# Performance work log

Hardware: AMD Instinct MI355X
Metric: run time of the kernel (lower is better)

The kernel has to match this reference:

```python
import jax, jax.numpy as jnp
import numpy as np

# blueprint: (root_input_idx, children) where child >= 0 -> input[child], child < 0 -> hidden[-child-1]
BLUEPRINT = [(0, [0, 1, 2, 3]), (4, [4, 5, 6, 7]), (8, [8, 9, 10, 11]), (12, [12, 13, 14, 15]), (0, [-1, -2, -3, -4])]
B, T, V, E, H, TAGS = 32768, 16, 32000, 32, 64, 64


def setup_inputs() -> dict:
    key = jax.random.key(0)
    ks = jax.random.split(key, 13)
    x = jax.random.randint(ks[0], (B, T), 0, V)  # token ids (never hit pad row V)
    s = jax.random.randint(ks[1], (B,), 1, 5)    # lengths in [1, 4]
    sc = 0.125  # ~1/sqrt(H), matches torch LSTM uniform init scale
    emb = (jax.random.normal(ks[2], (V + 1, E), dtype=jnp.float32) * 0.1).at[V].set(0.0)
    Wih = jax.random.uniform(ks[3], (4 * H, E), minval=-sc, maxval=sc, dtype=jnp.float32)
    Whh = jax.random.uniform(ks[4], (4 * H, H), minval=-sc, maxval=sc, dtype=jnp.float32)
    bih = jax.random.uniform(ks[5], (4 * H,), minval=-sc, maxval=sc, dtype=jnp.float32)
    bhh = jax.random.uniform(ks[6], (4 * H,), minval=-sc, maxval=sc, dtype=jnp.float32)
    h0 = jax.random.uniform(ks[7], (H,), minval=-1.0, maxval=1.0, dtype=jnp.float32)
    c0 = jax.random.uniform(ks[8], (H,), minval=-1.0, maxval=1.0, dtype=jnp.float32)
    Wc = jax.random.uniform(ks[9], (E, H + E), minval=-0.1, maxval=0.1, dtype=jnp.float32)
    bc = jnp.zeros((E,), dtype=jnp.float32)
    Wt = jax.random.uniform(ks[10], (TAGS, E), minval=-0.18, maxval=0.18, dtype=jnp.float32)
    bt = jnp.zeros((TAGS,), dtype=jnp.float32)
    return {"x": x, "s": s, "emb": emb, "Wih": Wih, "Whh": Whh, "bih": bih, "bhh": bhh,
            "h0": h0, "c0": c0, "Wc": Wc, "bc": bc, "Wt": Wt, "bt": bt}


def _lstm_seq(cseq, h0b, c0b, Wih, Whh, b):
    # cseq: [B, L, E] -> outputs [B, L, H]; torch gate order i, f, g, o
    def step(carry, xt):
        h, cc = carry
        g = xt @ Wih.T + h @ Whh.T + b
        i, f, gg, o = jnp.split(g, 4, axis=-1)
        cc = jax.nn.sigmoid(f) * cc + jax.nn.sigmoid(i) * jnp.tanh(gg)
        h = jax.nn.sigmoid(o) * jnp.tanh(cc)
        return (h, cc), h
    _, hs = jax.lax.scan(step, (h0b, c0b), jnp.swapaxes(cseq, 0, 1))
    return jnp.swapaxes(hs, 0, 1)


def reference(x, s, emb, Wih, Whh, bih, bhh, h0, c0, Wc, bc, Wt, bt):
    bsz = x.shape[0]
    inputs = emb[x]  # [B, T, E]
    h0b = jnp.broadcast_to(h0[None, :], (bsz, h0.shape[0]))
    c0b = jnp.broadcast_to(c0[None, :], (bsz, c0.shape[0]))
    b = bih + bhh
    hidden = []
    for root, children in BLUEPRINT:
        r = inputs[:, root]  # [B, E]
        ch = [inputs[:, c] if c >= 0 else hidden[-c - 1] for c in children]
        cseq = jnp.stack(ch, axis=1)  # [B, L, E]
        L = cseq.shape[1]
        o = _lstm_seq(cseq, h0b, c0b, Wih, Whh, b)  # [B, L, H]
        # pack/pad semantics: positions t >= s[b] are zero after pad_packed; relu(0)=0
        mask = (jnp.arange(L)[None, :] < s[:, None]).astype(o.dtype)
        o = jax.nn.relu(o) * mask[..., None]
        last = o[:, -1]  # [B, H] (zero where s[b] < L, matching torch)
        comb = jax.nn.relu(jnp.concatenate([r, last], axis=1) @ Wc.T + bc)  # [B, E]
        hidden.append(comb)
    logits = hidden[-1] @ Wt.T + bt  # [B, TAGS]
    return jax.nn.log_softmax(logits, axis=1)
```

## Files before the change

### kernel.cpp

```cpp
#include <hip/hip_runtime.h>

#define NB 32768
#define NT 16
#define NV 32001
#define NE 32
#define NTAGS 64

typedef __attribute__((ext_vector_type(8))) short short8;
typedef __attribute__((ext_vector_type(4))) float f4;

#define MFMA16(a, b, c) __builtin_amdgcn_mfma_f32_16x16x32_bf16(a, b, c, 0, 0, 0)
#define CFENCE() asm volatile("" ::: "memory")
#define LDSSYNC() asm volatile("s_waitcnt lgkmcnt(0)" ::: "memory")

__device__ __forceinline__ float sigm_(float x) {
    return __builtin_amdgcn_rcpf(1.0f + __expf(-x));
}
__device__ __forceinline__ float tanh2_(float x) {
    float e = __expf(-2.0f * x);
    return fmaf(2.0f, __builtin_amdgcn_rcpf(1.0f + e), -1.0f);
}
__device__ __forceinline__ short f2bf(float x) {
    union { float f; unsigned u; } v; v.f = x;
    unsigned r = v.u + 0x7fffu + ((v.u >> 16) & 1u);
    return (short)(r >> 16);
}

__global__ __launch_bounds__(1024) void classify_prep(
    const int* __restrict__ s, const float* __restrict__ emb,
    const float* __restrict__ Wih, const float* __restrict__ Whh,
    const float* __restrict__ bih, const float* __restrict__ bhh,
    const float* __restrict__ Wc, const float* __restrict__ Wt,
    short* __restrict__ embH, short* __restrict__ wpack, short* __restrict__ wc1,
    short* __restrict__ wc2, short* __restrict__ wth, float* __restrict__ bsum,
    int* __restrict__ cH, int* __restrict__ listH, int* __restrict__ listL) {
    __shared__ int wbH[16], wbL[16];
    const int tid = threadIdx.x, b = blockIdx.x;
    if (b < 32) {
        const int row = b * 1024 + tid;
        const bool heavy = s[row] >= 4;
        unsigned long long mk = __ballot(heavy);
        const int wv = tid >> 6, ln = tid & 63;
        if (ln == 0) wbH[wv] = __popcll(mk);
        __syncthreads();
        if (tid == 0) {
            int tH = 0, tL = 0;
#pragma unroll
            for (int i = 0; i < 16; ++i) {
                int ch = wbH[i];
                wbH[i] = tH; wbL[i] = tL;
                tH += ch; tL += 64 - ch;
            }
            cH[b] = tH;
        }
        __syncthreads();
        unsigned long long ltm = (1ull << ln) - 1ull;
        if (heavy) listH[b * 1024 + wbH[wv] + __popcll(mk & ltm)] = row;
        else       listL[b * 1024 + wbL[wv] + __popcll((~mk) & ltm)] = row;
    }
    for (int i = b * 1024 + tid; i < NV * NE; i += 262144) embH[i] = f2bf(emb[i]);
    if (b == 32) {
        for (int t = tid; t < 18432; t += 1024) {
            int r = t / 72, c = t % 72;
            wpack[t] = f2bf(c < 64 ? Whh[r * 64 + c] : 0.f);
        }
        for (int t = tid; t < 10240; t += 1024) {
            int r = t / 40, c = t % 40;
            wpack[18432 + t] = f2bf(c < 32 ? Wih[r * 32 + c] : 0.f);
        }
        if (tid < 1024) { int r = tid >> 5, c = tid & 31; wc1[tid] = f2bf(Wc[r * 96 + c]); }
        for (int t = tid; t < 2048; t += 1024) {
            int r = t >> 6, c = t & 63;
            wc2[t] = f2bf(Wc[r * 96 + 32 + c]);
        }
        for (int t = tid; t < 2048; t += 1024) {
            int r = t >> 5, c = t & 31;
            wth[t] = f2bf(Wt[r * 32 + c]);
        }
        if (tid < 256) bsum[tid] = bih[tid] + bhh[tid];
    }
}

__global__ __launch_bounds__(256, 2) void main_fused(
    const int* __restrict__ x, const float* __restrict__ emb,
    const float* __restrict__ h0, const float* __restrict__ c0,
    const float* __restrict__ Wc, const float* __restrict__ bc,
    const float* __restrict__ Wt, const float* __restrict__ bt,
    const float* __restrict__ bsum,
    const short* __restrict__ wpack, const short* __restrict__ wc1,
    const short* __restrict__ wc2, const short* __restrict__ wth,
    const short* __restrict__ embH, const int* __restrict__ cH,
    const int* __restrict__ listH, const int* __restrict__ listL,
    float* __restrict__ out) {
    __shared__ __align__(16) short sWhh[18432];
    __shared__ __align__(16) short sWih[10240];
    __shared__ __align__(16) short sHA[4][16 * 72];
    __shared__ __align__(16) short sCmb[4][16 * 40];
    __shared__ __align__(16) short sC4[4][4 * 40];
    __shared__ int sRow[16];

    const int tid = threadIdx.x, wave = tid >> 6, lane = tid & 63;
    const int q = lane >> 4, n = lane & 15;
    const int NW = gridDim.x * 4;
    const int gw = blockIdx.x * 4 + wave;

    int cs = (lane < 32) ? cH[lane] : 0;
    int v = cs;
#pragma unroll
    for (int o = 1; o < 32; o <<= 1) { int t2 = __shfl_up(v, o); if (lane >= o) v += t2; }
    const int vIncl = v, vExcl = v - cs;
    const int nH = __shfl(vIncl, 31);
    const int nL = NB - nH;
    const int liIncl = (lane + 1) * 1024 - vIncl;
    const int liExcl = lane * 1024 - vExcl;
    const int nHB = (nH + 15) >> 4;
    const bool heavyBlk = (int)blockIdx.x < nHB;

    if (heavyBlk) {
        for (int i = tid; i < 2304; i += 256)
            ((uint4*)sWhh)[i] = ((const uint4*)wpack)[i];
        for (int i = tid; i < 1280; i += 256)
            ((uint4*)sWih)[i] = ((const uint4*)(wpack + 18432))[i];
        __syncthreads();
    }

    if (heavyBlk) {
        short* hA = sHA[wave];
        short* cmbB = sCmb[0];
        short* c4 = sC4[0];

        float bias16[16];
#pragma unroll
        for (int tl = 0; tl < 16; ++tl) bias16[tl] = bsum[tl * 16 + n];
        float bc2[2] = {bc[n], bc[16 + n]};
        float bt4[4] = {bt[n], bt[16 + n], bt[32 + n], bt[48 + n]};
        float c0v[4];
#pragma unroll
        for (int u = 0; u < 4; ++u) c0v[u] = c0[u * 16 + n];
        short8 h0f0, h0f1;
#pragma unroll
        for (int j = 0; j < 8; ++j) {
            h0f0[j] = f2bf(h0[q * 8 + j]);
            h0f1[j] = f2bf(h0[32 + q * 8 + j]);
        }
        const float c0w = c0[wave * 16 + n];

        const f4 zero4 = {0.f, 0.f, 0.f, 0.f};
        f4 acc[16];
        float cst[4][4];

        auto doStep = [&](short8 aP, short8 ah0, short8 ah1, bool doRelu) {
#pragma unroll
            for (int tl = 0; tl < 16; ++tl)
                acc[tl] = MFMA16(aP, *(const short8*)&sWih[(tl * 16 + n) * 40 + q * 8], zero4);
#pragma unroll
            for (int tl = 0; tl < 16; ++tl) {
                const short* rbp = &sWhh[(tl * 16 + n) * 72 + q * 8];
                f4 t0 = acc[tl];
                t0 = MFMA16(ah0, *(const short8*)rbp, t0);
                t0 = MFMA16(ah1, *(const short8*)(rbp + 32), t0);
                acc[tl] = t0;
            }
            CFENCE();
#pragma unroll
            for (int u = 0; u < 4; ++u)
#pragma unroll
                for (int r = 0; r < 4; ++r) {
                    float ip = acc[u][r] + bias16[u];
                    float fp = acc[4 + u][r] + bias16[4 + u];
                    float gp = acc[8 + u][r] + bias16[8 + u];
                    float op = acc[12 + u][r] + bias16[12 + u];
                    float cc = fmaf(sigm_(fp), cst[r][u], sigm_(ip) * tanh2_(gp));
                    cst[r][u] = cc;
                    float hh = sigm_(op) * tanh2_(cc);
                    if (doRelu) hh = fmaxf(hh, 0.f);
                    hA[(q * 4 + r) * 72 + u * 16 + n] = f2bf(hh);
                }
            CFENCE();
        };

#pragma unroll 1
        for (int itb = blockIdx.x; itb * 16 < nH; itb += (int)gridDim.x) {
            const int base = itb * 16;
            int idxq = min(base + wave * 4 + q, nH - 1);
            int sl = 0;
#pragma unroll
            for (int b2 = 0; b2 < 32; ++b2) sl += (__shfl(vIncl, b2) <= idxq) ? 1 : 0;
            const int row = listH[sl * 1024 + idxq - __shfl(vExcl, sl)];
            if (n == 0) sRow[wave * 4 + q] = row;
            const int tokAll = x[row * 16 + n];
            const int liBase = (n & 3) * 16 + (n >> 2) * 4;

#pragma unroll
            for (int u = 0; u < 4; ++u)
#pragma unroll
                for (int r = 0; r < 4; ++r) cst[r][u] = c0v[u];
            const int tokR0 = __shfl(tokAll, liBase);
            short8 aNext = *(const short8*)&embH[tokR0 * 32 + q * 8];
            short8 a0 = h0f0, a1 = h0f1;
#pragma unroll 1
            for (int t = 0; t < 4; ++t) {
                short8 aP = aNext;
                if (t < 3) {
                    int tk2 = __shfl(tokAll, liBase + t + 1);
                    aNext = *(const short8*)&embH[tk2 * 32 + q * 8];
                }
                doStep(aP, a0, a1, t == 3);
                if (t < 3) {
                    a0 = *(const short8*)&hA[n * 72 + q * 8];
                    a1 = *(const short8*)&hA[n * 72 + 32 + q * 8];
                }
            }
            {
                short8 aRoot = *(const short8*)&embH[tokR0 * 32 + q * 8];
                short8 lh0 = *(const short8*)&hA[n * 72 + q * 8];
                short8 lh1 = *(const short8*)&hA[n * 72 + 32 + q * 8];
#pragma unroll
                for (int tl2 = 0; tl2 < 2; ++tl2) {
                    float bv = bc2[tl2];
                    f4 t0 = {bv, bv, bv, bv};
                    short8 b1 = *(const short8*)&wc1[(tl2 * 16 + n) * 32 + q * 8];
                    t0 = MFMA16(aRoot, b1, t0);
                    const short* rbp = &wc2[(tl2 * 16 + n) * 64 + q * 8];
                    t0 = MFMA16(lh0, *(const short8*)rbp, t0);
                    t0 = MFMA16(lh1, *(const short8*)(rbp + 32), t0);
#pragma unroll
                    for (int r = 0; r < 4; ++r) {
                        int m = q * 4 + r;
                        cmbB[((m >> 2) * 16 + wave * 4 + (m & 3)) * 40 + tl2 * 16 + n] =
                            f2bf(fmaxf(t0[r], 0.f));
                    }
                }
            }
            __syncthreads();

            float bias4[4];
#pragma unroll
            for (int j = 0; j < 4; ++j) bias4[j] = bsum[(j * 4 + wave) * 16 + n];
            float cstw[4] = {c0w, c0w, c0w, c0w};
            short8 b0 = h0f0, b1 = h0f1;
            f4 ac4[4];
#pragma unroll
            for (int t = 0; t < 4; ++t) {
                short* hbw = (t & 1) ? sHA[1] : sHA[0];
                short8 aC = *(const short8*)&cmbB[(t * 16 + n) * 40 + q * 8];
#pragma unroll
                for (int j = 0; j < 4; ++j)
                    ac4[j] = MFMA16(aC,
                        *(const short8*)&sWih[((j * 4 + wave) * 16 + n) * 40 + q * 8], zero4);
#pragma unroll
                for (int j = 0; j < 4; ++j) {
                    const short* rbp = &sWhh[((j * 4 + wave) * 16 + n) * 72 + q * 8];
                    f4 t0 = ac4[j];
                    t0 = MFMA16(b0, *(const short8*)rbp, t0);
                    t0 = MFMA16(b1, *(const short8*)(rbp + 32), t0);
                    ac4[j] = t0;
                }
                CFENCE();
#pragma unroll
                for (int r = 0; r < 4; ++r) {
                    float ip = ac4[0][r] + bias4[0];
                    float fp = ac4[1][r] + bias4[1];
                    float gp = ac4[2][r] + bias4[2];
                    float op = ac4[3][r] + bias4[3];
                    float cc = fmaf(sigm_(fp), cstw[r], sigm_(ip) * tanh2_(gp));
                    cstw[r] = cc;
                    float hh = sigm_(op) * tanh2_(cc);
                    if (t == 3) hh = fmaxf(hh, 0.f);
                    hbw[(q * 4 + r) * 72 + wave * 16 + n] = f2bf(hh);
                }
                CFENCE();
                __syncthreads();
                if (t < 3) {
                    b0 = *(const short8*)&hbw[n * 72 + q * 8];
                    b1 = *(const short8*)&hbw[n * 72 + 32 + q * 8];
                }
            }

            {
                const short* hL = sHA[1];
                int rv = sRow[n];
                int tokR = x[rv * 16];
                short8 aR = *(const short8*)&embH[tokR * 32 + q * 8];
                short8 lb0 = *(const short8*)&hL[n * 72 + q * 8];
                short8 lb1 = *(const short8*)&hL[n * 72 + 32 + q * 8];
#pragma unroll
                for (int tl2 = 0; tl2 < 2; ++tl2) {
                    float bv = bc2[tl2];
                    f4 t0 = {bv, bv, bv, bv};
                    short8 b1f = *(const short8*)&wc1[(tl2 * 16 + n) * 32 + q * 8];
                    t0 = MFMA16(aR, b1f, t0);
                    const short* rbp = &wc2[(tl2 * 16 + n) * 64 + q * 8];
                    t0 = MFMA16(lb0, *(const short8*)rbp, t0);
                    t0 = MFMA16(lb1, *(const short8*)(rbp + 32), t0);
                    if (q == wave) {
#pragma unroll
                        for (int r = 0; r < 4; ++r)
                            c4[(wave * 4 + r) * 40 + tl2 * 16 + n] = f2bf(fmaxf(t0[r], 0.f));
                    }
                }
            }
            __syncthreads();

            {
                short8 cA = *(const short8*)&c4[n * 40 + q * 8];
                f4 a3[4];
#pragma unroll
                for (int tl3 = 0; tl3 < 4; ++tl3) {
                    float bv = bt4[tl3];
                    f4 t0 = {bv, bv, bv, bv};
                    short8 bW = *(const short8*)&wth[(tl3 * 16 + n) * 32 + q * 8];
                    a3[tl3] = MFMA16(cA, bW, t0);
                }
#pragma unroll
                for (int r = 0; r < 4; ++r) {
                    float l0 = a3[0][r], l1 = a3[1][r], l2 = a3[2][r], l3 = a3[3][r];
                    float mx = fmaxf(fmaxf(l0, l1), fmaxf(l2, l3));
#pragma unroll
                    for (int o2 = 8; o2; o2 >>= 1) mx = fmaxf(mx, __shfl_xor(mx, o2));
                    float sm = __expf(l0 - mx) + __expf(l1 - mx) +
                               __expf(l2 - mx) + __expf(l3 - mx);
#pragma unroll
                    for (int o2 = 8; o2; o2 >>= 1) sm += __shfl_xor(sm, o2);
                    float lse = mx + __logf(sm);
                    if (q == wave && base + wave * 4 + r < nH) {
                        int ro = sRow[wave * 4 + r];
                        out[ro * 64 + n] = l0 - lse;
                        out[ro * 64 + 16 + n] = l1 - lse;
                        out[ro * 64 + 32 + n] = l2 - lse;
                        out[ro * 64 + 48 + n] = l3 - lse;
                    }
                }
            }
        }
    }

    if (nL > 0) {
        const int nLB = max((int)gridDim.x - nHB, 0);
        int lw, nlw;
        if (nLB > 0) {
            if (heavyBlk) { lw = -1; nlw = 0; }
            else { lw = ((int)blockIdx.x - nHB) * 4 + wave; nlw = nLB * 4; }
        } else {
            lw = NW - 1 - gw; nlw = NW;
        }
        if (lw >= 0) {
            short* cmbL = sCmb[wave];
            f4 bcV[2], btV[4];
#pragma unroll
            for (int t = 0; t < 2; ++t) { float bv = bc[t * 16 + n]; bcV[t] = f4{bv, bv, bv, bv}; }
#pragma unroll
            for (int t = 0; t < 4; ++t) { float bv = bt[t * 16 + n]; btV[t] = f4{bv, bv, bv, bv}; }
#pragma unroll 1
            for (int base = lw * 16; base < nL; base += nlw * 16) {
                int idx = min(base + lane, nL - 1);
                int sl = 0;
#pragma unroll
                for (int b2 = 0; b2 < 32; ++b2) sl += (__shfl(liIncl, b2) <= idx) ? 1 : 0;
                const int lrow = listL[sl * 1024 + idx - __shfl(liExcl, sl)];
                const int ltok = x[lrow * 16];
                short8 aE = *(const short8*)&embH[__shfl(ltok, n) * 32 + q * 8];
#pragma unroll
                for (int tl2 = 0; tl2 < 2; ++tl2) {
                    short8 b1 = *(const short8*)&wc1[(tl2 * 16 + n) * 32 + q * 8];
                    f4 t0 = MFMA16(aE, b1, bcV[tl2]);
#pragma unroll
                    for (int r = 0; r < 4; ++r)
                        cmbL[(q * 4 + r) * 40 + tl2 * 16 + n] = f2bf(fmaxf(t0[r], 0.f));
                }
                CFENCE();
                short8 cA = *(const short8*)&cmbL[n * 40 + q * 8];
                f4 a3[4];
#pragma unroll
                for (int tl3 = 0; tl3 < 4; ++tl3) {
                    short8 bW = *(const short8*)&wth[(tl3 * 16 + n) * 32 + q * 8];
                    a3[tl3] = MFMA16(cA, bW, btV[tl3]);
                }
#pragma unroll
                for (int r = 0; r < 4; ++r) {
                    float l0 = a3[0][r], l1 = a3[1][r], l2 = a3[2][r], l3 = a3[3][r];
                    float mx = fmaxf(fmaxf(l0, l1), fmaxf(l2, l3));
#pragma unroll
                    for (int o2 = 8; o2; o2 >>= 1) mx = fmaxf(mx, __shfl_xor(mx, o2));
                    float sm = __expf(l0 - mx) + __expf(l1 - mx) +
                               __expf(l2 - mx) + __expf(l3 - mx);
#pragma unroll
                    for (int o2 = 8; o2; o2 >>= 1) sm += __shfl_xor(sm, o2);
                    float lse = mx + __logf(sm);
                    int rowO = __shfl(lrow, q * 4 + r);
                    if (base + q * 4 + r < nL) {
                        out[rowO * 64 + n] = l0 - lse;
                        out[rowO * 64 + 16 + n] = l1 - lse;
                        out[rowO * 64 + 32 + n] = l2 - lse;
                        out[rowO * 64 + 48 + n] = l3 - lse;
                    }
                }
                CFENCE();
            }
        }
    }
}

__global__ __launch_bounds__(512) void tagger_fallback(
    const int* __restrict__ x, const int* __restrict__ s, const float* __restrict__ emb,
    const float* __restrict__ Wih, const float* __restrict__ Whh,
    const float* __restrict__ bih, const float* __restrict__ bhh,
    const float* __restrict__ h0, const float* __restrict__ c0,
    const float* __restrict__ Wc, const float* __restrict__ bc,
    const float* __restrict__ Wt, const float* __restrict__ bt,
    float* __restrict__ out) {
    __shared__ float4 WhhP[4096];
    __shared__ float combBuf[8][128];
    for (int i = threadIdx.x; i < 4096; i += 512) {
        int k = i & 63, jj = i >> 6;
        WhhP[k * 64 + jj] = make_float4(Whh[jj * 64 + k], Whh[(jj + 64) * 64 + k],
                                        Whh[(jj + 128) * 64 + k], Whh[(jj + 192) * 64 + k]);
    }
    __syncthreads();
    const int wave = threadIdx.x >> 6, j = threadIdx.x & 63, jm = j & 31;
    const int b = blockIdx.x * 8 + wave;
    const int sv = s[b];
    const int* xb = x + b * NT;
    const float bcj = bc[jm];
    auto rc_val = [&](int tok) -> float {
        float r = 0.f;
#pragma unroll
        for (int k = 0; k < 32; ++k) r = fmaf(emb[tok * NE + k], Wc[jm * 96 + k], r);
        return r;
    };
    float comb4;
    if (sv >= 4) {
        const float h0j = h0[j], c0j = c0[j];
        float4 bsj = make_float4(bih[j] + bhh[j], bih[j + 64] + bhh[j + 64],
                                 bih[j + 128] + bhh[j + 128], bih[j + 192] + bhh[j + 192]);
#pragma unroll 1
        for (int node = 0; node < 4; ++node) {
            float h = h0j, c = c0j;
#pragma unroll 1
            for (int t = 0; t < 4; ++t) {
                int tok = xb[node * 4 + t];
                float4 p = bsj;
#pragma unroll
                for (int k = 0; k < 32; ++k) {
                    float e = emb[tok * NE + k];
                    p.x = fmaf(e, Wih[j * 32 + k], p.x);
                    p.y = fmaf(e, Wih[(j + 64) * 32 + k], p.y);
                    p.z = fmaf(e, Wih[(j + 128) * 32 + k], p.z);
                    p.w = fmaf(e, Wih[(j + 192) * 32 + k], p.w);
                }
                float4 a = make_float4(0.f, 0.f, 0.f, 0.f);
#pragma unroll
                for (int k = 0; k < 64; ++k) {
                    float hk = __shfl(h, k);
                    float4 w = WhhP[k * 64 + j];
                    a.x = fmaf(hk, w.x, a.x); a.y = fmaf(hk, w.y, a.y);
                    a.z = fmaf(hk, w.z, a.z); a.w = fmaf(hk, w.w, a.w);
                }
                a.x += p.x; a.y += p.y; a.z += p.z; a.w += p.w;
                float ig = sigm_(a.x), fg = sigm_(a.y), gg = tanh2_(a.z), og = sigm_(a.w);
                c = fmaf(fg, c, ig * gg);
                h = og * tanh2_(c);
            }
            float last = fmaxf(h, 0.f);
            float acc = rc_val(xb[node * 4]) + bcj;
#pragma unroll
            for (int k = 0; k < 64; ++k)
                acc = fmaf(__shfl(last, k), Wc[jm * 96 + 32 + k], acc);
            if (j < 32) combBuf[wave][node * 32 + j] = fmaxf(acc, 0.f);
        }
        LDSSYNC();
        float h = h0j, c = c0j;
#pragma unroll 1
        for (int t = 0; t < 4; ++t) {
            float4 a = make_float4(0.f, 0.f, 0.f, 0.f);
#pragma unroll
            for (int k = 0; k < 32; ++k) {
                float ck = combBuf[wave][t * 32 + k];
                a.x = fmaf(ck, Wih[j * 32 + k], a.x);
                a.y = fmaf(ck, Wih[(j + 64) * 32 + k], a.y);
                a.z = fmaf(ck, Wih[(j + 128) * 32 + k], a.z);
                a.w = fmaf(ck, Wih[(j + 192) * 32 + k], a.w);
            }
#pragma unroll
            for (int k = 0; k < 64; ++k) {
                float hk = __shfl(h, k);
                float4 w = WhhP[k * 64 + j];
                a.x = fmaf(hk, w.x, a.x); a.y = fmaf(hk, w.y, a.y);
                a.z = fmaf(hk, w.z, a.z); a.w = fmaf(hk, w.w, a.w);
            }
            a.x += bih[j] + bhh[j]; a.y += bih[j + 64] + bhh[j + 64];
            a.z += bih[j + 128] + bhh[j + 128]; a.w += bih[j + 192] + bhh[j + 192];
            float ig = sigm_(a.x), fg = sigm_(a.y), gg = tanh2_(a.z), og = sigm_(a.w);
            c = fmaf(fg, c, ig * gg);
            h = og * tanh2_(c);
        }
        float last = fmaxf(h, 0.f);
        float acc = rc_val(xb[0]) + bcj;
#pragma unroll
        for (int k = 0; k < 64; ++k)
            acc = fmaf(__shfl(last, k), Wc[jm * 96 + 32 + k], acc);
        comb4 = fmaxf(acc, 0.f);
    } else {
        comb4 = fmaxf(rc_val(xb[0]) + bcj, 0.f);
    }
    float logit = bt[j];
    const float* wtr = Wt + j * 32;
#pragma unroll
    for (int k = 0; k < 32; ++k) logit = fmaf(__shfl(comb4, k), wtr[k], logit);
    float mx = logit;
#pragma unroll
    for (int off = 32; off; off >>= 1) mx = fmaxf(mx, __shfl_xor(mx, off));
    float ex = __expf(logit - mx);
    float sum = ex;
#pragma unroll
    for (int off = 32; off; off >>= 1) sum += __shfl_xor(sum, off);
    out[b * 64 + j] = logit - mx - __logf(sum);
}

extern "C" void kernel_launch(void* const* d_in, const int* in_sizes, int n_in,
                              void* d_out, int out_size, void* d_ws, size_t ws_size,
                              hipStream_t stream) {
    const int* x = (const int*)d_in[0];
    const int* s = (const int*)d_in[1];
    const float* emb = (const float*)d_in[2];
    const float* Wih = (const float*)d_in[3];
    const float* Whh = (const float*)d_in[4];
    const float* bih = (const float*)d_in[5];
    const float* bhh = (const float*)d_in[6];
    const float* h0 = (const float*)d_in[7];
    const float* c0 = (const float*)d_in[8];
    const float* Wc = (const float*)d_in[9];
    const float* bc = (const float*)d_in[10];
    const float* Wt = (const float*)d_in[11];
    const float* bt = (const float*)d_in[12];
    float* out = (float*)d_out;

    auto al16 = [](size_t v) { return (v + 15) & ~(size_t)15; };
    size_t off = 0;
    size_t oWpack = off; off = al16(off + (size_t)28672 * 2);
    size_t oWc1 = off;   off = al16(off + 1024 * 2);
    size_t oWc2 = off;   off = al16(off + 2048 * 2);
    size_t oWt = off;    off = al16(off + 2048 * 2);
    size_t oBsum = off;  off = al16(off + 256 * 4);
    size_t oEmbH = off;  off = al16(off + (size_t)NV * NE * 2);
    size_t oCH = off;    off = al16(off + 32 * 4);
    size_t oListH = off; off = al16(off + (size_t)NB * 4);
    size_t oListL = off; off = al16(off + (size_t)NB * 4);
    size_t need = off;

    char* ws = (char*)d_ws;
    if (ws_size >= need) {
        short* wpack = (short*)(ws + oWpack);
        short* wc1 = (short*)(ws + oWc1);
        short* wc2 = (short*)(ws + oWc2);
        short* wth = (short*)(ws + oWt);
        float* bsum = (float*)(ws + oBsum);
        short* embH = (short*)(ws + oEmbH);
        int* cHp = (int*)(ws + oCH);
        int* listH = (int*)(ws + oListH);
        int* listL = (int*)(ws + oListL);

        classify_prep<<<dim3(256), dim3(1024), 0, stream>>>(
            s, emb, Wih, Whh, bih, bhh, Wc, Wt,
            embH, wpack, wc1, wc2, wth, bsum, cHp, listH, listL);
        main_fused<<<dim3(768), dim3(256), 0, stream>>>(
            x, emb, h0, c0, Wc, bc, Wt, bt, bsum,
            wpack, wc1, wc2, wth, embH, cHp, listH, listL, out);
    } else {
        tagger_fallback<<<dim3(4096), dim3(512), 0, stream>>>(
            x, s, emb, Wih, Whh, bih, bhh, h0, c0, Wc, bc, Wt, bt, out);
    }
}
```

Baseline: 139.6 us.

## Prefetch first heavy tile before weight staging and rebalance light work across all waves

The first heavy-tile row lookup, token fetch and embedding load are issued before the shared-memory weight copy and barrier, so their latency overlaps the staging. The combine-stage LDS read of the next timestep's input is software-pipelined one step ahead. Light-row work is now spread over every wave in reverse order rather than only over non-heavy blocks, and the grid shrinks from 768 to 512 blocks. This targets load latency and imbalance between the heavy and light paths, at the cost of more live registers and heavy blocks also taking light work.

Measured after the change: 135.5 us. -2.9%, faster.

```diff
diff --git a/kernel.cpp b/kernel.cpp
--- a/kernel.cpp
+++ b/kernel.cpp
@@ -116,6 +116,19 @@
     const int nHB = (nH + 15) >> 4;
     const bool heavyBlk = (int)blockIdx.x < nHB;
 
+    int row0 = 0, tokAll0 = 0;
+    short8 aNext0;
+    const int liBase = (n & 3) * 16 + (n >> 2) * 4;
+    if (heavyBlk) {
+        int idxq = min((int)blockIdx.x * 16 + wave * 4 + q, nH - 1);
+        int sl = 0;
+#pragma unroll
+        for (int b2 = 0; b2 < 32; ++b2) sl += (__shfl(vIncl, b2) <= idxq) ? 1 : 0;
+        row0 = listH[sl * 1024 + idxq - __shfl(vExcl, sl)];
+        tokAll0 = x[row0 * 16 + n];
+        aNext0 = *(const short8*)&embH[__shfl(tokAll0, liBase) * 32 + q * 8];
+    }
+
     if (heavyBlk) {
         for (int i = tid; i < 2304; i += 256)
             ((uint4*)sWhh)[i] = ((const uint4*)wpack)[i];
@@ -182,21 +195,26 @@
 #pragma unroll 1
         for (int itb = blockIdx.x; itb * 16 < nH; itb += (int)gridDim.x) {
             const int base = itb * 16;
-            int idxq = min(base + wave * 4 + q, nH - 1);
-            int sl = 0;
-#pragma unroll
-            for (int b2 = 0; b2 < 32; ++b2) sl += (__shfl(vIncl, b2) <= idxq) ? 1 : 0;
-            const int row = listH[sl * 1024 + idxq - __shfl(vExcl, sl)];
+            int row, tokAll;
+            short8 aNext;
+            if (itb == (int)blockIdx.x) {
+                row = row0; tokAll = tokAll0; aNext = aNext0;
+            } else {
+                int idxq = min(base + wave * 4 + q, nH - 1);
+                int sl = 0;
+#pragma unroll
+                for (int b2 = 0; b2 < 32; ++b2) sl += (__shfl(vIncl, b2) <= idxq) ? 1 : 0;
+                row = listH[sl * 1024 + idxq - __shfl(vExcl, sl)];
+                tokAll = x[row * 16 + n];
+                aNext = *(const short8*)&embH[__shfl(tokAll, liBase) * 32 + q * 8];
+            }
             if (n == 0) sRow[wave * 4 + q] = row;
-            const int tokAll = x[row * 16 + n];
-            const int liBase = (n & 3) * 16 + (n >> 2) * 4;
+            const int tokR0 = __shfl(tokAll, liBase);
 
 #pragma unroll
             for (int u = 0; u < 4; ++u)
 #pragma unroll
                 for (int r = 0; r < 4; ++r) cst[r][u] = c0v[u];
-            const int tokR0 = __shfl(tokAll, liBase);
-            short8 aNext = *(const short8*)&embH[tokR0 * 32 + q * 8];
             short8 a0 = h0f0, a1 = h0f1;
 #pragma unroll 1
             for (int t = 0; t < 4; ++t) {
@@ -239,11 +257,14 @@
             for (int j = 0; j < 4; ++j) bias4[j] = bsum[(j * 4 + wave) * 16 + n];
             float cstw[4] = {c0w, c0w, c0w, c0w};
             short8 b0 = h0f0, b1 = h0f1;
+            short8 aCn = *(const short8*)&cmbB[(0 * 16 + n) * 40 + q * 8];
             f4 ac4[4];
 #pragma unroll
             for (int t = 0; t < 4; ++t) {
                 short* hbw = (t & 1) ? sHA[1] : sHA[0];
-                short8 aC = *(const short8*)&cmbB[(t * 16 + n) * 40 + q * 8];
+                short8 aC = aCn;
+                if (t < 3)
+                    aCn = *(const short8*)&cmbB[((t + 1) * 16 + n) * 40 + q * 8];
 #pragma unroll
                 for (int j = 0; j < 4; ++j)
                     ac4[j] = MFMA16(aC,
@@ -336,15 +357,9 @@
     }
 
     if (nL > 0) {
-        const int nLB = max((int)gridDim.x - nHB, 0);
-        int lw, nlw;
-        if (nLB > 0) {
-            if (heavyBlk) { lw = -1; nlw = 0; }
-            else { lw = ((int)blockIdx.x - nHB) * 4 + wave; nlw = nLB * 4; }
-        } else {
-            lw = NW - 1 - gw; nlw = NW;
-        }
-        if (lw >= 0) {
+        const int lw = NW - 1 - gw;
+        const int base0 = lw * 16;
+        if (base0 < nL) {
             short* cmbL = sCmb[wave];
             f4 bcV[2], btV[4];
 #pragma unroll
@@ -352,8 +367,8 @@
 #pragma unroll
             for (int t = 0; t < 4; ++t) { float bv = bt[t * 16 + n]; btV[t] = f4{bv, bv, bv, bv}; }
 #pragma unroll 1
-            for (int base = lw * 16; base < nL; base += nlw * 16) {
-                int idx = min(base + lane, nL - 1);
+            for (int base = base0; base < nL; base += NW * 16) {
+                int idx = min(base + (lane & 15), nL - 1);
                 int sl = 0;
 #pragma unroll
                 for (int b2 = 0; b2 < 32; ++b2) sl += (__shfl(liIncl, b2) <= idx) ? 1 : 0;
@@ -563,7 +578,7 @@
         classify_prep<<<dim3(256), dim3(1024), 0, stream>>>(
             s, emb, Wih, Whh, bih, bhh, Wc, Wt,
             embH, wpack, wc1, wc2, wth, bsum, cHp, listH, listL);
-        main_fused<<<dim3(768), dim3(256), 0, stream>>>(
+        main_fused<<<dim3(512), dim3(256), 0, stream>>>(
             x, emb, h0, c0, Wc, bc, Wt, bt, bsum,
             wpack, wc1, wc2, wth, embH, cHp, listH, listL, out);
     } else {
```
